# Kernel tuning notes

Measured on AMD Instinct MI355X. Metric: run time of the kernel, lower is better.

## Reference

```python
import jax, jax.numpy as jnp
import numpy as np

B, C, L, D, H = 8, 64, 128, 768, 768  # batch, candidates, tokens, hidden, mlp hidden


def setup_inputs() -> dict:
    key = jax.random.key(0)
    k0, k1, k2 = jax.random.split(key, 3)
    inp = jax.random.normal(k0, (B, C, 2, L, D), dtype=jnp.float32)
    # MlpModule params (input_size = 768*2): Linear(2D->H) -> ReLU -> Linear(H->1)
    W1 = jax.random.normal(k1, (2 * D, H), dtype=jnp.float32) * 0.02
    b1 = jnp.zeros((H,), dtype=jnp.float32)
    W2 = jax.random.normal(k2, (H, 1), dtype=jnp.float32) * 0.02
    b2 = jnp.zeros((1,), dtype=jnp.float32)
    return {"input": inp, "W1": W1, "b1": b1, "W2": W2, "b2": b2}


def reference(input, W1, b1, W2, b2):
    b, c, _, l, d = input.shape
    context = input[:, :, 0].reshape(b * c, l, d)  # [BC, L, D]
    entity = input[:, :, 1].reshape(b * c, l, d)   # [BC, L, D]
    mask = (context[:, :, 0] != 0).astype(context.dtype)  # [BC, L]

    # bmm similarity: [BC, L, L]
    sim = jnp.einsum('bld,bmd->blm', context, entity)
    dot_scores = jnp.max(sim, axis=-1)          # [BC, L]
    argmax_values = jnp.argmax(sim, axis=-1)    # [BC, L]

    # gather best-matching entity token per context token: [BC, L, D]
    gathered = jnp.take_along_axis(entity, argmax_values[..., None], axis=1)

    # MLP over stacked (context, entity) pair -> flatten to 2D features
    mlp_in = jnp.concatenate([context, gathered], axis=-1)  # [BC, L, 2D]
    h = jax.nn.relu(mlp_in @ W1 + b1)
    scores = (h @ W2 + b2)[..., 0]              # [BC, L]

    scores = jnp.sum(scores * mask, axis=-1)              # [BC]
    dot_scores = jnp.sum(dot_scores * mask, axis=-1).reshape(b, c)  # [B, C]
    return scores, dot_scores
```

## Files before the change

### kernel.cpp

```cpp
#include <hip/hip_runtime.h>
#include <hip/hip_bf16.h>
#include <stdint.h>

#define NPAIR 512
#define LTOK  128
#define DDIM  768
#define HDIM  768
#define K2    1536
#define MARGIN 0.4f

typedef float f32x4 __attribute__((ext_vector_type(4)));
typedef short bf16x8 __attribute__((ext_vector_type(8)));

static __device__ __forceinline__ unsigned short f2bf(float f) {
    union { float f; uint32_t u; } v; v.f = f;
    uint32_t u = v.u;
    u += 0x7FFF + ((u >> 16) & 1);
    return (unsigned short)(u >> 16);
}

static __device__ __forceinline__ uint2 pack4(f32x4 v) {
    __hip_bfloat162 lo = __float22bfloat162_rn(float2{v[0], v[1]});
    __hip_bfloat162 hi = __float22bfloat162_rn(float2{v[2], v[3]});
    uint2 r;
    r.x = *reinterpret_cast<unsigned*>(&lo);
    r.y = *reinterpret_cast<unsigned*>(&hi);
    return r;
}

typedef const __attribute__((address_space(1))) void* gas_t;
typedef __attribute__((address_space(3))) void* las_t;
static __device__ __forceinline__ void gld16(const void* g, void* l) {
    __builtin_amdgcn_global_load_lds((gas_t)g, (las_t)l, 16, 0, 0);
}

static __device__ __forceinline__ float wave_dot(const float* __restrict__ a,
                                                 const float* __restrict__ b,
                                                 int lane) {
    f32x4 s4 = {0.f, 0.f, 0.f, 0.f};
#pragma unroll
    for (int it = 0; it < 3; ++it) {
        int k = it * 256 + lane * 4;
        f32x4 av = *(const f32x4*)(a + k);
        f32x4 bv = *(const f32x4*)(b + k);
#pragma unroll
        for (int q = 0; q < 4; ++q) s4[q] = fmaf(av[q], bv[q], s4[q]);
    }
    float v = (s4[0] + s4[1]) + (s4[2] + s4[3]);
#pragma unroll
    for (int m = 1; m < 64; m <<= 1) v += __shfl_xor(v, m);
    return v;
}

__global__ __launch_bounds__(256, 2) void simfma_kernel(
        const float* __restrict__ inp,
        float* __restrict__ dotmax, int* __restrict__ argmax,
        unsigned short* __restrict__ Cbf, unsigned short* __restrict__ Ebf)
{
    const int p    = blockIdx.x;
    const int t    = threadIdx.x;
    const int wv   = t >> 6;
    const int lane = t & 63;
    const int s    = lane & 15, g = lane >> 4;

    const float* Cbase = inp + (size_t)(2 * p) * LTOK * DDIM;
    const float* Ebase = Cbase + (size_t)LTOK * DDIM;

    __shared__ unsigned short Cl[2][128][32];
    __shared__ unsigned short El[2][128][32];
    __shared__ unsigned short cand[128][16];
    __shared__ int   ccnt[128];
    __shared__ float rm1[128];
    __shared__ int   ri1[128];

    if (t < 128) ccnt[t] = 0;

    f32x4 acc[2][8];
#pragma unroll
    for (int i = 0; i < 2; i++)
#pragma unroll
        for (int j = 0; j < 8; j++) acc[i][j] = (f32x4){0.f, 0.f, 0.f, 0.f};

    for (int kc = 0; kc < 12; ++kc) {
        const int k0 = kc * 64;
#pragma unroll
        for (int it = 0; it < 8; ++it) {
            int slot = it * 256 + t;
            int row = slot >> 4, l16 = slot & 15;
            int h = l16 >> 3, kl = (l16 & 7) * 4;
            f32x4 cv = *(const f32x4*)(Cbase + (size_t)row * DDIM + k0 + l16 * 4);
            uint2 cw = pack4(cv);
            *(uint2*)&Cl[h][row][kl] = cw;
            *(uint2*)(Cbf + ((size_t)p * LTOK + row) * DDIM + k0 + l16 * 4) = cw;
        }
#pragma unroll
        for (int it = 0; it < 8; ++it) {
            int slot = it * 256 + t;
            int row = slot >> 4, l16 = slot & 15;
            int h = l16 >> 3, kl = (l16 & 7) * 4;
            f32x4 ev = *(const f32x4*)(Ebase + (size_t)row * DDIM + k0 + l16 * 4);
            uint2 ew = pack4(ev);
            *(uint2*)&El[h][row][kl] = ew;
            *(uint2*)(Ebf + ((size_t)p * LTOK + row) * DDIM + k0 + l16 * 4) = ew;
        }
        __syncthreads();

#pragma unroll
        for (int h = 0; h < 2; ++h) {
            bf16x8 af[2], bfr[8];
#pragma unroll
            for (int i = 0; i < 2; ++i)
                af[i] = *(const bf16x8*)&Cl[h][wv * 32 + i * 16 + s][g * 8];
#pragma unroll
            for (int j = 0; j < 8; ++j)
                bfr[j] = *(const bf16x8*)&El[h][j * 16 + s][g * 8];
#pragma unroll
            for (int i = 0; i < 2; ++i)
#pragma unroll
                for (int j = 0; j < 8; ++j)
                    acc[i][j] = __builtin_amdgcn_mfma_f32_16x16x32_bf16(af[i], bfr[j], acc[i][j], 0, 0, 0);
        }
        __syncthreads();
    }

#pragma unroll
    for (int i = 0; i < 2; ++i)
#pragma unroll
        for (int r = 0; r < 4; ++r) {
            float m1 = acc[i][0][r]; int i1 = s; float m2 = -1e30f;
#pragma unroll
            for (int j = 1; j < 8; ++j) {
                float v = acc[i][j][r]; int c = j * 16 + s;
                if (v > m1 || (v == m1 && c < i1)) { m2 = m1; m1 = v; i1 = c; }
                else if (v > m2) m2 = v;
            }
#pragma unroll
            for (int msk = 1; msk < 16; msk <<= 1) {
                float o1 = __shfl_xor(m1, msk);
                int   oi = __shfl_xor(i1, msk);
                float o2 = __shfl_xor(m2, msk);
                bool take = (o1 > m1) || (o1 == m1 && oi < i1);
                float nm2 = take ? fmaxf(m1, o2) : fmaxf(m2, o1);
                if (take) { m1 = o1; i1 = oi; }
                m2 = nm2;
            }
            int row = wv * 32 + i * 16 + g * 4 + r;
            if (s == 0) { rm1[row] = m1; ri1[row] = i1; }
            float thr = m1 - MARGIN;
#pragma unroll
            for (int j = 0; j < 8; ++j) {
                float v = acc[i][j][r]; int c = j * 16 + s;
                if (v >= thr && c != i1) {
                    int idx = atomicAdd(&ccnt[row], 1);
                    if (idx < 16) cand[row][idx] = (unsigned short)c;
                }
            }
        }
    __syncthreads();

    for (int rr = 0; rr < 32; ++rr) {
        int row = wv + rr * 4;
        int cnt = ccnt[row];
        float m1 = rm1[row]; int i1 = ri1[row];
        size_t ob = (size_t)p * LTOK + row;
        if (cnt == 0) {
            if (lane == 0) { dotmax[ob] = m1; argmax[ob] = i1; }
            continue;
        }
        const float* cr = Cbase + (size_t)row * DDIM;
        float bv; int bc;
        if (cnt <= 16) {
            bv = wave_dot(cr, Ebase + (size_t)i1 * DDIM, lane); bc = i1;
            for (int q = 0; q < cnt; ++q) {
                int c = cand[row][q];
                float v = wave_dot(cr, Ebase + (size_t)c * DDIM, lane);
                if (v > bv || (v == bv && c < bc)) { bv = v; bc = c; }
            }
        } else {
            bv = -1e30f; bc = 0;
            for (int c = 0; c < 128; ++c) {
                float v = wave_dot(cr, Ebase + (size_t)c * DDIM, lane);
                if (v > bv || (v == bv && c < bc)) { bv = v; bc = c; }
            }
        }
        if (lane == 0) { dotmax[ob] = bv; argmax[ob] = bc; }
    }
}

__global__ __launch_bounds__(256) void w1t_kernel(
        const float* __restrict__ W1, unsigned short* __restrict__ W1T)
{
    int idx = blockIdx.x * 256 + threadIdx.x;
    if (idx >= HDIM * K2 / 8) return;
    int c  = idx / (K2 / 8);
    int k0 = (idx % (K2 / 8)) * 8;
    unsigned short v[8];
#pragma unroll
    for (int q = 0; q < 8; q++) v[q] = f2bf(W1[(size_t)(k0 + q) * HDIM + c]);
    *(uint4*)(W1T + (size_t)c * K2 + k0) = *(const uint4*)v;
}

__global__ __launch_bounds__(256, 2) void mlp2_kernel(
        const unsigned short* __restrict__ Cbf,
        const unsigned short* __restrict__ Ebf,
        const unsigned short* __restrict__ W1T,
        const float* __restrict__ b1,
        const float* __restrict__ W2,
        const int* __restrict__ argmax,
        float* __restrict__ part)
{
    const int p    = blockIdx.x;
    const int cbk  = blockIdx.y;
    const int t    = threadIdx.x;
    const int wv   = t >> 6;
    const int lane = t & 63;
    const int s    = lane & 15, g = lane >> 4;
    const int wr   = wv >> 1, wc = wv & 1;

    __shared__ unsigned short Ald[2][128][32];
    __shared__ unsigned short Bld[2][256][32];
    __shared__ int am[128];

    if (t < 128) am[t] = argmax[p * LTOK + t];

    f32x4 acc[4][8];
#pragma unroll
    for (int i = 0; i < 4; i++)
#pragma unroll
        for (int j = 0; j < 8; j++) acc[i][j] = (f32x4){0.f, 0.f, 0.f, 0.f};

    const int rsub = lane >> 2;
    const int chk  = lane & 3;

    auto STAGE = [&](int buf, int kt) {
        const int k0   = kt * 32;
        const bool ctx = (kt < 24);
        const int kloc = ctx ? k0 : (k0 - DDIM);
#pragma unroll
        for (int n = 0; n < 4; ++n) {
            int c0  = (wv * 4 + n) * 16;
            int col = c0 + rsub;
            gld16(W1T + (size_t)(cbk * 256 + col) * K2 + k0 + chk * 8,
                  &Bld[buf][c0][0]);
        }
#pragma unroll
        for (int n = 0; n < 2; ++n) {
            int r0 = (wv * 2 + n) * 16;
            int r  = r0 + rsub;
            const unsigned short* base = ctx
                ? (Cbf + ((size_t)p * LTOK + r) * DDIM)
                : (Ebf + ((size_t)p * LTOK + am[r]) * DDIM);
            gld16(base + kloc + chk * 8, &Ald[buf][r0][0]);
        }
    };

    STAGE(0, 0);
    __syncthreads();

    int cur = 0;
    for (int kt = 0; kt < 47; ++kt) {
        STAGE(cur ^ 1, kt + 1);
        bf16x8 af[4], bfr[8];
#pragma unroll
        for (int i = 0; i < 4; ++i)
            af[i] = *(const bf16x8*)&Ald[cur][wr * 64 + i * 16 + s][g * 8];
#pragma unroll
        for (int j = 0; j < 8; ++j)
            bfr[j] = *(const bf16x8*)&Bld[cur][wc * 128 + j * 16 + s][g * 8];
#pragma unroll
        for (int i = 0; i < 4; ++i)
#pragma unroll
            for (int j = 0; j < 8; ++j)
                acc[i][j] = __builtin_amdgcn_mfma_f32_16x16x32_bf16(af[i], bfr[j], acc[i][j], 0, 0, 0);
        __syncthreads();
        cur ^= 1;
    }
    {
        bf16x8 af[4], bfr[8];
#pragma unroll
        for (int i = 0; i < 4; ++i)
            af[i] = *(const bf16x8*)&Ald[cur][wr * 64 + i * 16 + s][g * 8];
#pragma unroll
        for (int j = 0; j < 8; ++j)
            bfr[j] = *(const bf16x8*)&Bld[cur][wc * 128 + j * 16 + s][g * 8];
#pragma unroll
        for (int i = 0; i < 4; ++i)
#pragma unroll
            for (int j = 0; j < 8; ++j)
                acc[i][j] = __builtin_amdgcn_mfma_f32_16x16x32_bf16(af[i], bfr[j], acc[i][j], 0, 0, 0);
    }

    float w2v[8], b1v[8];
#pragma unroll
    for (int j = 0; j < 8; j++) {
        int col = cbk * 256 + wc * 128 + j * 16 + s;
        w2v[j] = W2[col];
        b1v[j] = b1[col];
    }
    float ssum[4][4];
#pragma unroll
    for (int i = 0; i < 4; i++)
#pragma unroll
        for (int r = 0; r < 4; r++) ssum[i][r] = 0.f;
#pragma unroll
    for (int i = 0; i < 4; i++)
#pragma unroll
        for (int j = 0; j < 8; j++)
#pragma unroll
            for (int r = 0; r < 4; r++) {
                float h = acc[i][j][r] + b1v[j];
                h = h > 0.f ? h : 0.f;
                ssum[i][r] = fmaf(h, w2v[j], ssum[i][r]);
            }
#pragma unroll
    for (int sft = 1; sft < 16; sft <<= 1)
#pragma unroll
        for (int i = 0; i < 4; i++)
#pragma unroll
            for (int r = 0; r < 4; r++) ssum[i][r] += __shfl_xor(ssum[i][r], sft);
    if (s == 0) {
        const int q = cbk * 2 + wc;
#pragma unroll
        for (int i = 0; i < 4; i++)
#pragma unroll
            for (int r = 0; r < 4; r++)
                part[(size_t)q * (NPAIR * LTOK) + p * LTOK + wr * 64 + i * 16 + g * 4 + r]
                    = ssum[i][r];
    }
}

__global__ __launch_bounds__(128) void reduce6_kernel(
        const float* __restrict__ inp,
        const float* __restrict__ part,
        const float* __restrict__ dotmax,
        const float* __restrict__ b2,
        float* __restrict__ out)
{
    int p = blockIdx.x;
    int l = threadIdx.x;
    float c0  = inp[((size_t)(2 * p) * LTOK + l) * DDIM];
    float msk = (c0 != 0.0f) ? 1.f : 0.f;
    float sc = b2[0];
#pragma unroll
    for (int q = 0; q < 6; ++q)
        sc += part[(size_t)q * (NPAIR * LTOK) + p * LTOK + l];
    sc *= msk;
    float dm = dotmax[p * LTOK + l] * msk;
#pragma unroll
    for (int sh = 1; sh < 64; sh <<= 1) {
        sc += __shfl_xor(sc, sh);
        dm += __shfl_xor(dm, sh);
    }
    __shared__ float tmp[4];
    if ((l & 63) == 0) { tmp[(l >> 6) * 2] = sc; tmp[(l >> 6) * 2 + 1] = dm; }
    __syncthreads();
    if (l == 0) {
        out[p]          = tmp[0] + tmp[2];
        out[NPAIR + p]  = tmp[1] + tmp[3];
    }
}

__global__ __launch_bounds__(256) void sim_fp32_kernel(
        const float* __restrict__ inp,
        float* __restrict__ dotmax, int* __restrict__ argmax)
{
    const int p  = blockIdx.x;
    const int t  = threadIdx.x;
    const int tx = t & 15, ty = t >> 4;
    const float* Cbase = inp + (size_t)(2 * p) * LTOK * DDIM;
    const float* Ebase = Cbase + (size_t)LTOK * DDIM;

    __shared__ float Ct[128][36];
    __shared__ float Et[128][36];

    float acc[8][8];
#pragma unroll
    for (int i = 0; i < 8; i++)
#pragma unroll
        for (int j = 0; j < 8; j++) acc[i][j] = 0.f;

    for (int kc = 0; kc < 24; ++kc) {
        const int k0 = kc * 32;
#pragma unroll
        for (int q = 0; q < 4; ++q) {
            int f = q * 256 + t;
            int row = f >> 3, c4 = f & 7;
            *(f32x4*)&Ct[row][c4 * 4] = *(const f32x4*)(Cbase + (size_t)row * DDIM + k0 + c4 * 4);
            *(f32x4*)&Et[row][c4 * 4] = *(const f32x4*)(Ebase + (size_t)row * DDIM + k0 + c4 * 4);
        }
        __syncthreads();
#pragma unroll
        for (int kk4 = 0; kk4 < 8; ++kk4) {
            f32x4 cr[8], er[8];
#pragma unroll
            for (int i = 0; i < 8; i++) cr[i] = *(const f32x4*)&Ct[ty + 16 * i][kk4 * 4];
#pragma unroll
            for (int j = 0; j < 8; j++) er[j] = *(const f32x4*)&Et[tx + 16 * j][kk4 * 4];
#pragma unroll
            for (int kk = 0; kk < 4; kk++)
#pragma unroll
                for (int i = 0; i < 8; i++)
#pragma unroll
                    for (int j = 0; j < 8; j++)
                        acc[i][j] = fmaf(cr[i][kk], er[j][kk], acc[i][j]);
        }
        __syncthreads();
    }
#pragma unroll
    for (int i = 0; i < 8; i++) {
        float m = acc[i][0]; int mi = tx;
#pragma unroll
        for (int j = 1; j < 8; j++) {
            int c = tx + 16 * j;
            float v = acc[i][j];
            if (v > m || (v == m && c < mi)) { m = v; mi = c; }
        }
#pragma unroll
        for (int sft = 1; sft < 16; sft <<= 1) {
            float vo = __shfl_xor(m, sft);
            int   io = __shfl_xor(mi, sft);
            if (vo > m || (vo == m && io < mi)) { m = vo; mi = io; }
        }
        if (tx == 0) {
            int r = ty + 16 * i;
            dotmax[(size_t)p * LTOK + r] = m;
            argmax[(size_t)p * LTOK + r] = mi;
        }
    }
}

__global__ __launch_bounds__(256, 2) void mlp_kernel(
        const float* __restrict__ inp,
        const unsigned short* __restrict__ W1T,
        const float* __restrict__ b1,
        const float* __restrict__ W2,
        const int* __restrict__ argmax,
        float* __restrict__ tokscore)
{
    const int tile = blockIdx.x;
    const int cb   = blockIdx.y;
    const int t    = threadIdx.x;
    const int wv   = t >> 6;
    const int lane = t & 63;
    const int s    = lane & 15, g = lane >> 4;

    __shared__ unsigned short At[64][32];
    __shared__ unsigned short Bt[384][32];
    __shared__ int am[64];

    if (t < 64) am[t] = argmax[tile * 64 + t];
    __syncthreads();

    f32x4 acc[4][6];
#pragma unroll
    for (int i = 0; i < 4; i++)
#pragma unroll
        for (int j = 0; j < 6; j++) acc[i][j] = (f32x4){0.f, 0.f, 0.f, 0.f};

    for (int kc = 0; kc < 48; ++kc) {
        const int k0  = kc * 32;
        const int sel = (kc >= 24) ? 1 : 0;
        const int kloc = k0 - sel * DDIM;
#pragma unroll
        for (int q = 0; q < 2; ++q) {
            int f = q * 256 + t;
            int row = f >> 3, c4 = f & 7;
            int token = tile * 64 + row;
            int pp = token >> 7;
            int lsel = sel ? am[row] : (token & 127);
            const float* src = inp + ((size_t)(2 * pp + sel) * LTOK + lsel) * DDIM + kloc + c4 * 4;
            f32x4 v = *(const f32x4*)src;
            uint2 pk = pack4(v);
            *(uint2*)&At[row][c4 * 4] = pk;
        }
#pragma unroll
        for (int q = 0; q < 6; ++q) {
            int f = q * 256 + t;
            int colr = f >> 2, q8 = f & 3;
            const unsigned short* src = W1T + (size_t)(cb * 384 + colr) * K2 + k0 + q8 * 8;
            *(uint4*)&Bt[colr][q8 * 8] = *(const uint4*)src;
        }
        __syncthreads();

        bf16x8 af[4], bfr[6];
#pragma unroll
        for (int i = 0; i < 4; i++) af[i]  = *(const bf16x8*)&At[i * 16 + s][g * 8];
#pragma unroll
        for (int j = 0; j < 6; j++) bfr[j] = *(const bf16x8*)&Bt[wv * 96 + j * 16 + s][g * 8];
#pragma unroll
        for (int i = 0; i < 4; i++)
#pragma unroll
            for (int j = 0; j < 6; j++)
                acc[i][j] = __builtin_amdgcn_mfma_f32_16x16x32_bf16(af[i], bfr[j], acc[i][j], 0, 0, 0);
        __syncthreads();
    }

    float w2v[6], b1v[6];
#pragma unroll
    for (int j = 0; j < 6; j++) {
        int col = cb * 384 + wv * 96 + j * 16 + s;
        w2v[j] = W2[col];
        b1v[j] = b1[col];
    }
    float ssum[4][4];
#pragma unroll
    for (int i = 0; i < 4; i++)
#pragma unroll
        for (int r = 0; r < 4; r++) ssum[i][r] = 0.f;
#pragma unroll
    for (int i = 0; i < 4; i++)
#pragma unroll
        for (int j = 0; j < 6; j++)
#pragma unroll
            for (int r = 0; r < 4; r++) {
                float h = acc[i][j][r] + b1v[j];
                h = h > 0.f ? h : 0.f;
                ssum[i][r] = fmaf(h, w2v[j], ssum[i][r]);
            }
#pragma unroll
    for (int sft = 1; sft < 16; sft <<= 1)
#pragma unroll
        for (int i = 0; i < 4; i++)
#pragma unroll
            for (int r = 0; r < 4; r++) ssum[i][r] += __shfl_xor(ssum[i][r], sft);
    if (s == 0) {
#pragma unroll
        for (int i = 0; i < 4; i++)
#pragma unroll
            for (int r = 0; r < 4; r++)
                atomicAdd(&tokscore[tile * 64 + i * 16 + g * 4 + r], ssum[i][r]);
    }
}

__global__ __launch_bounds__(128) void reduce_kernel(
        const float* __restrict__ inp,
        const float* __restrict__ tokscore,
        const float* __restrict__ dotmax,
        const float* __restrict__ b2,
        float* __restrict__ out)
{
    int p = blockIdx.x;
    int l = threadIdx.x;
    float c0  = inp[((size_t)(2 * p) * LTOK + l) * DDIM];
    float msk = (c0 != 0.0f) ? 1.f : 0.f;
    float sc  = (tokscore[p * LTOK + l] + b2[0]) * msk;
    float dm  = dotmax[p * LTOK + l] * msk;
#pragma unroll
    for (int sh = 1; sh < 64; sh <<= 1) {
        sc += __shfl_xor(sc, sh);
        dm += __shfl_xor(dm, sh);
    }
    __shared__ float tmp[4];
    if ((l & 63) == 0) { tmp[(l >> 6) * 2] = sc; tmp[(l >> 6) * 2 + 1] = dm; }
    __syncthreads();
    if (l == 0) {
        out[p]          = tmp[0] + tmp[2];
        out[NPAIR + p]  = tmp[1] + tmp[3];
    }
}

extern "C" void kernel_launch(void* const* d_in, const int* in_sizes, int n_in,
                              void* d_out, int out_size, void* d_ws, size_t ws_size,
                              hipStream_t stream)
{
    const float* inp = (const float*)d_in[0];
    const float* W1  = (const float*)d_in[1];
    const float* b1  = (const float*)d_in[2];
    const float* W2  = (const float*)d_in[3];
    const float* b2  = (const float*)d_in[4];
    float* out = (float*)d_out;

    char* ws = (char*)d_ws;
    unsigned short* W1T   = (unsigned short*)ws;
    float*          dotmx = (float*)(ws + 2359296);
    int*            amax  = (int*)(ws + 2359296 + 262144);
    float*          toksc = (float*)(ws + 2359296 + 2*262144);
    unsigned short* Cbf   = (unsigned short*)(ws + 2359296 + 3*262144);
    unsigned short* Ebf   = Cbf + (size_t)NPAIR * LTOK * DDIM;
    float*          part  = (float*)(ws + 2359296 + 3*262144 + 2*100663296ull);
    const size_t NEED = 2359296ull + 3ull*262144ull + 2ull*100663296ull + 6ull*262144ull;

    const bool big = ws_size >= NEED;

    w1t_kernel<<<(HDIM * K2 / 8 + 255) / 256, 256, 0, stream>>>(W1, W1T);
    if (big) {
        simfma_kernel<<<NPAIR, 256, 0, stream>>>(inp, dotmx, amax, Cbf, Ebf);
        mlp2_kernel<<<dim3(NPAIR, 3), 256, 0, stream>>>(Cbf, Ebf, W1T, b1, W2, amax, part);
        reduce6_kernel<<<NPAIR, 128, 0, stream>>>(inp, part, dotmx, b2, out);
    } else {
        hipMemsetAsync(toksc, 0, 65536 * sizeof(float), stream);
        sim_fp32_kernel<<<NPAIR, 256, 0, stream>>>(inp, dotmx, amax);
        mlp_kernel<<<dim3(1024, 2), 256, 0, stream>>>(inp, W1T, b1, W2, amax, toksc);
        reduce_kernel<<<NPAIR, 128, 0, stream>>>(inp, toksc, dotmx, b2, out);
    }
}
```

Measured before the change: 328.9 us.

## Prefetch next fp32 chunk into registers during MFMA and widen stores to 16B

Global fp32 loads for the next k-chunk now go into registers before the current chunk's MFMAs run, so load latency overlaps with compute. Each thread now handles 8 contiguous floats and writes 16-byte bf16 packets to LDS and to the global bf16 copies instead of 8-byte ones. The global bf16 stores are moved after the barrier. This costs 64 extra VGPRs of prefetch buffers, which may lower occupancy.

```diff
diff --git a/kernel.cpp b/kernel.cpp
--- a/kernel.cpp
+++ b/kernel.cpp
@@ -28,6 +28,12 @@
     return r;
 }
 
+static __device__ __forceinline__ uint4 pack8(f32x4 a, f32x4 b) {
+    uint2 lo = pack4(a), hi = pack4(b);
+    uint4 r; r.x = lo.x; r.y = lo.y; r.z = hi.x; r.w = hi.y;
+    return r;
+}
+
 typedef const __attribute__((address_space(1))) void* gas_t;
 typedef __attribute__((address_space(3))) void* las_t;
 static __device__ __forceinline__ void gld16(const void* g, void* l) {
@@ -81,29 +87,47 @@
 #pragma unroll
         for (int j = 0; j < 8; j++) acc[i][j] = (f32x4){0.f, 0.f, 0.f, 0.f};
 
+    const int srow[4] = { (0*256 + t) >> 3, (1*256 + t) >> 3,
+                          (2*256 + t) >> 3, (3*256 + t) >> 3 };
+    const int so8 = t & 7;
+    const int sh  = so8 >> 2;
+    const int skl = (so8 & 3) * 8;
+
+    f32x4 cbuf[8], ebuf[8];
+
+    auto ISSUE = [&](int kc) {
+        const int k0 = kc * 64;
+#pragma unroll
+        for (int it = 0; it < 4; ++it) {
+            const float* ca = Cbase + (size_t)srow[it] * DDIM + k0 + so8 * 8;
+            const float* ea = Ebase + (size_t)srow[it] * DDIM + k0 + so8 * 8;
+            cbuf[it * 2]     = *(const f32x4*)ca;
+            cbuf[it * 2 + 1] = *(const f32x4*)(ca + 4);
+            ebuf[it * 2]     = *(const f32x4*)ea;
+            ebuf[it * 2 + 1] = *(const f32x4*)(ea + 4);
+        }
+    };
+
+    ISSUE(0);
     for (int kc = 0; kc < 12; ++kc) {
         const int k0 = kc * 64;
-#pragma unroll
-        for (int it = 0; it < 8; ++it) {
-            int slot = it * 256 + t;
-            int row = slot >> 4, l16 = slot & 15;
-            int h = l16 >> 3, kl = (l16 & 7) * 4;
-            f32x4 cv = *(const f32x4*)(Cbase + (size_t)row * DDIM + k0 + l16 * 4);
-            uint2 cw = pack4(cv);
-            *(uint2*)&Cl[h][row][kl] = cw;
-            *(uint2*)(Cbf + ((size_t)p * LTOK + row) * DDIM + k0 + l16 * 4) = cw;
-        }
-#pragma unroll
-        for (int it = 0; it < 8; ++it) {
-            int slot = it * 256 + t;
-            int row = slot >> 4, l16 = slot & 15;
-            int h = l16 >> 3, kl = (l16 & 7) * 4;
-            f32x4 ev = *(const f32x4*)(Ebase + (size_t)row * DDIM + k0 + l16 * 4);
-            uint2 ew = pack4(ev);
-            *(uint2*)&El[h][row][kl] = ew;
-            *(uint2*)(Ebf + ((size_t)p * LTOK + row) * DDIM + k0 + l16 * 4) = ew;
+        uint4 cw[4], ew[4];
+#pragma unroll
+        for (int it = 0; it < 4; ++it) {
+            cw[it] = pack8(cbuf[it * 2], cbuf[it * 2 + 1]);
+            ew[it] = pack8(ebuf[it * 2], ebuf[it * 2 + 1]);
+            *(uint4*)&Cl[sh][srow[it]][skl] = cw[it];
+            *(uint4*)&El[sh][srow[it]][skl] = ew[it];
         }
         __syncthreads();
+
+        if (kc < 11) ISSUE(kc + 1);
+#pragma unroll
+        for (int it = 0; it < 4; ++it) {
+            size_t off = ((size_t)p * LTOK + srow[it]) * DDIM + k0 + so8 * 8;
+            *(uint4*)(Cbf + off) = cw[it];
+            *(uint4*)(Ebf + off) = ew[it];
+        }
 
 #pragma unroll
         for (int h = 0; h < 2; ++h) {
```

New measurement: 330.3 us. No clear change (+0.4%).
